# Kernel optimization log

Hardware: AMD Instinct MI355X
Metric: run time of the kernel (lower is better)

Reference implementation:

```python
import jax, jax.numpy as jnp
import numpy as np

# 'tetra_chiral' permutation table from the original module
_TETRA_CHIRAL = np.array([
    [0, 1, 2, 3], [0, 2, 3, 1], [0, 3, 1, 2], [1, 0, 3, 2],
    [1, 2, 0, 3], [1, 3, 2, 0], [2, 0, 1, 3], [2, 1, 3, 0],
    [2, 3, 0, 1], [3, 0, 2, 1], [3, 1, 0, 2], [3, 2, 1, 0]], dtype=np.int32)

N, H = 65536, 256
BN_EPS = 1e-5


def setup_inputs() -> dict:
    key = jax.random.key(0)
    ks = jax.random.split(key, 6)
    x = jax.random.normal(ks[0], (N, 4, H), dtype=jnp.float32)
    # 4 hidden x hidden linears (xavier-ish scale), stacked [4, H, H] (torch weight layout: [out, in])
    Wb = jax.random.normal(ks[1], (4, H, H), dtype=jnp.float32) * (1.0 / np.sqrt(H))
    bb = jnp.zeros((4, H), dtype=jnp.float32)
    W1 = jax.random.normal(ks[2], (H, H), dtype=jnp.float32) * (1.0 / np.sqrt(H))
    b1 = jnp.zeros((H,), dtype=jnp.float32)
    gamma = jnp.ones((H,), dtype=jnp.float32)
    beta = jnp.zeros((H,), dtype=jnp.float32)
    W2 = jax.random.normal(ks[3], (H, H), dtype=jnp.float32) * (1.0 / np.sqrt(H))
    b2 = jnp.zeros((H,), dtype=jnp.float32)
    perms = jnp.asarray(_TETRA_CHIRAL)
    return {"x": x, "Wb": Wb, "bb": bb, "W1": W1, "b1": b1,
            "gamma": gamma, "beta": beta, "W2": W2, "b2": b2, "perms": perms}


def reference(x, Wb, bb, W1, b1, gamma, beta, W2, b2, perms):
    # x: [N, 4, H]; perms: [P, 4] with P=12 (tetra_chiral)
    # For each permutation p: relu(sum_k tanh(Linear_k(x[:, p[k], :]))), accumulated over p.
    acc = jnp.zeros((x.shape[0], perms.shape[0], x.shape[2]), dtype=x.dtype)  # [N, P, H]
    for k in range(4):  # fixed tiny loop over the 4 slot-linears
        xs = x[:, perms[:, k], :]  # gather: [N, P, H]
        acc = acc + jnp.tanh(jnp.einsum('nph,gh->npg', xs, Wb[k]) + bb[k])
    nei = jnp.maximum(acc, 0.0).sum(axis=1)  # relu per perm, sum over perms -> [N, H]
    # mlp_out: Linear -> BatchNorm1d(eval: mean=0, var=1) -> ReLU -> Linear
    z = (nei / 3.0) @ W1.T + b1
    inv = jnp.float32(1.0 / np.sqrt(1.0 + BN_EPS))
    h = jnp.maximum(z * inv * gamma + beta, 0.0)
    return h @ W2.T + b2
```

## Files before the change

### kernel.cpp

```cpp
#include <hip/hip_runtime.h>
#include <cstdint>
#include <cstddef>

typedef __bf16 bf16x8 __attribute__((ext_vector_type(8)));
typedef float  f32x16 __attribute__((ext_vector_type(16)));
typedef float  f32x2  __attribute__((ext_vector_type(2)));

__device__ __forceinline__ unsigned f2bf_u(float f){
  unsigned u = __float_as_uint(f);
  return (u + 0x7FFFu + ((u >> 16) & 1u)) >> 16;
}
__device__ __forceinline__ unsigned short f2bf(float f){ return (unsigned short)f2bf_u(f); }

__device__ __forceinline__ f32x2 tanh2v(f32x2 x){
  f32x2 e2 = x * 2.8853900817779268f;
  f32x2 e  = { __builtin_amdgcn_exp2f(e2.x), __builtin_amdgcn_exp2f(e2.y) };
  f32x2 d  = e + 1.0f;
  f32x2 r  = { __builtin_amdgcn_rcpf(d.x), __builtin_amdgcn_rcpf(d.y) };
  return 1.0f - 2.0f * r;
}

#define MFMA(a,b,c) __builtin_amdgcn_mfma_f32_32x32x16_bf16((a),(b),(c),0,0,0)

__device__ __forceinline__ void ld_lds16(const void* g, void* l){
  __builtin_amdgcn_global_load_lds(
      (const __attribute__((address_space(1))) unsigned int*)g,
      (__attribute__((address_space(3))) unsigned int*)l, 16, 0, 0);
}
__device__ __forceinline__ bf16x8 mk_frag(uint2 lo, uint2 hi){
  return __builtin_bit_cast(bf16x8, make_uint4(lo.x, lo.y, hi.x, hi.y));
}

__global__ void prep_wb(const float* __restrict__ Wb, unsigned short* __restrict__ dst){
  int s  = blockIdx.x*256 + threadIdx.x;
  int r  = s & 31;
  int c  = (s>>5) & 3;
  int tj = (s>>7) & 3;
  int ks = (s>>9) & 3;
  int kq = (s>>11) & 3;
  int gc = (s>>13) & 7;
  const float* src = Wb + ((size_t)tj*256 + gc*32 + r)*256 + kq*64 + ks*16 + c*4;
  float4 f = *reinterpret_cast<const float4*>(src);
  ushort4 o; o.x=f2bf(f.x); o.y=f2bf(f.y); o.z=f2bf(f.z); o.w=f2bf(f.w);
  *reinterpret_cast<ushort4*>(dst + (size_t)s*4) = o;
}

__global__ void prep_w(const float* __restrict__ W1, const float* __restrict__ W2,
                       unsigned short* __restrict__ dst){
  int id = blockIdx.x*256 + threadIdx.x;
  const float* W = (id < 8192) ? W1 : W2;
  int s  = id & 8191;
  int l  = s & 63;
  int ks = (s>>6) & 15;
  int ct = (s>>10) & 7;
  const float* src = W + ((size_t)ct*32 + (l&31))*256 + ks*16 + (l>>5)*8;
  float4 f0 = *reinterpret_cast<const float4*>(src);
  float4 f1 = *reinterpret_cast<const float4*>(src + 4);
  ushort4 a, b;
  a.x=f2bf(f0.x); a.y=f2bf(f0.y); a.z=f2bf(f0.z); a.w=f2bf(f0.w);
  b.x=f2bf(f1.x); b.y=f2bf(f1.y); b.z=f2bf(f1.z); b.w=f2bf(f1.w);
  ushort4* d = reinterpret_cast<ushort4*>(dst + (size_t)id*8);
  d[0] = a; d[1] = b;
}

__launch_bounds__(256, 3)
__global__ void tetra_main(const float* __restrict__ x,
                           const float* __restrict__ bb,
                           const float* __restrict__ b1,
                           const float* __restrict__ gam,
                           const float* __restrict__ bet,
                           const float* __restrict__ b2,
                           const unsigned short* __restrict__ wsWb,
                           const unsigned short* __restrict__ wsW1,
                           const unsigned short* __restrict__ wsW2,
                           float* __restrict__ out)
{
  __shared__ __align__(16) uint2 sbuf[2][2048];
  __shared__ __align__(16) uint2 snei[2112];

  constexpr int PT[12][4] = {{0,1,2,3},{0,2,3,1},{0,3,1,2},{1,0,3,2},{1,2,0,3},{1,3,2,0},
                             {2,0,1,3},{2,1,3,0},{2,3,0,1},{3,0,2,1},{3,1,0,2},{3,2,1,0}};

  const int tid  = threadIdx.x;
  const int w    = tid >> 6;
  const int lane = tid & 63;
  const int l31  = lane & 31;
  const int q    = lane >> 5;

  uint4 fragA[16];
  {
    const float* arow = x + ((size_t)blockIdx.x*128 + (size_t)(w*32 + l31))*256 + q*8;
#pragma unroll
    for (int s = 0; s < 16; ++s){
      float4 f0 = *reinterpret_cast<const float4*>(arow + s*16);
      float4 f1 = *reinterpret_cast<const float4*>(arow + s*16 + 4);
      fragA[s] = make_uint4(f2bf_u(f0.x) | (f2bf_u(f0.y)<<16),
                            f2bf_u(f0.z) | (f2bf_u(f0.w)<<16),
                            f2bf_u(f1.x) | (f2bf_u(f1.y)<<16),
                            f2bf_u(f1.z) | (f2bf_u(f1.w)<<16));
    }
  }

  float bcur[4], bnext[4];
#pragma unroll
  for (int k = 0; k < 4; ++k) bcur[k] = bb[k*256 + l31];

  auto stage = [&](int t){
    const char* g = (const char*)wsWb + (size_t)t*16384 + w*4096 + lane*16;
    char* lb = (char*)(&sbuf[t&1][0]) + w*4096;
#pragma unroll
    for (int i = 0; i < 4; ++i)
      ld_lds16(g + i*1024, lb + i*1024);
  };

  stage(0);

  unsigned short* sn = (unsigned short*)snei;
  int t = 0;
  for (int gc = 0; gc < 8; ++gc){
    f32x16 acc[4];
#pragma unroll
    for (int k = 0; k < 4; ++k){
      float bv = bcur[k];
#pragma unroll
      for (int r = 0; r < 16; ++r) acc[k][r] = bv;
    }

#pragma unroll
    for (int kq = 0; kq < 4; ++kq, ++t){
      __syncthreads();
      if (t < 31) stage(t+1);
      const uint2* B = sbuf[t&1];
      const int boff = q*64 + l31;
#pragma unroll
      for (int ks = 0; ks < 4; ++ks){
        bf16x8 av = __builtin_bit_cast(bf16x8, fragA[kq*4 + ks]);
#pragma unroll
        for (int tj = 0; tj < 4; ++tj){
          int idx = (ks*16 + tj*4)*32 + boff;
          uint2 lo = B[idx], hi = B[idx + 32];
          acc[tj] = MFMA(av, mk_frag(lo, hi), acc[tj]);
        }
      }
    }

#pragma unroll
    for (int k = 0; k < 4; ++k) bnext[k] = bb[k*256 + ((gc+1)&7)*32 + l31];

    const int col   = gc*32 + l31;
    const int sbase = (col>>2)*132 + (col&3);
#pragma unroll
    for (int npair = 0; npair < 2; ++npair){
      const int nb0 = 2*npair, nb1 = nb0 + 1;
      f32x2 th[4][4];
#pragma unroll
      for (int k = 0; k < 4; ++k)
#pragma unroll
        for (int t2 = 0; t2 < 4; ++t2){
          f32x2 a = { acc[k][nb0*4 + t2], acc[k][nb1*4 + t2] };
          th[k][t2] = tanh2v(a);
        }
      float s0 = 0.0f, s1 = 0.0f;
#pragma unroll
      for (int p = 0; p < 12; ++p){
        f32x2 v = (th[0][PT[p][0]] + th[1][PT[p][1]])
                + (th[2][PT[p][2]] + th[3][PT[p][3]]);
        s0 += fmaxf(v.x, 0.0f);
        s1 += fmaxf(v.y, 0.0f);
      }
      sn[sbase + (w*8 + 2*nb0 + q)*4] = f2bf(s0 * (1.0f/3.0f));
      sn[sbase + (w*8 + 2*nb1 + q)*4] = f2bf(s1 * (1.0f/3.0f));
    }

#pragma unroll
    for (int k = 0; k < 4; ++k) bcur[k] = bnext[k];
  }

  float b1v0 = b1[(w*2+0)*32 + l31];
  float b1v1 = b1[(w*2+1)*32 + l31];
  __syncthreads();

  const int ct0 = w*2, ct1 = w*2 + 1;
  f32x16 a2[2];
#pragma unroll
  for (int r = 0; r < 16; ++r){ a2[0][r] = b1v0; a2[1][r] = b1v1; }
  {
    const uint4* W1f = (const uint4*)wsW1;
    uint4 bp[8][2];
#pragma unroll
    for (int i = 0; i < 8; ++i){
      bp[i][0] = W1f[(ct0*16 + i)*64 + lane];
      bp[i][1] = W1f[(ct1*16 + i)*64 + lane];
    }
#pragma unroll
    for (int ks = 0; ks < 16; ++ks){
      int ai = (ks*4 + q*2)*33 + l31;
      uint2 lo = snei[ai], hi = snei[ai + 33];
      bf16x8 av = mk_frag(lo, hi);
      uint4 c0 = bp[ks&7][0], c1 = bp[ks&7][1];
      if (ks < 8){
        bp[ks][0] = W1f[(ct0*16 + ks + 8)*64 + lane];
        bp[ks][1] = W1f[(ct1*16 + ks + 8)*64 + lane];
      }
      a2[0] = MFMA(av, __builtin_bit_cast(bf16x8, c0), a2[0]);
      a2[1] = MFMA(av, __builtin_bit_cast(bf16x8, c1), a2[1]);
    }
  }
  float gvv[2], btv[2], b2v[2];
#pragma unroll
  for (int tj = 0; tj < 2; ++tj){
    int colx = (w*2 + tj)*32 + l31;
    gvv[tj] = gam[colx]; btv[tj] = bet[colx]; b2v[tj] = b2[colx];
  }
  __syncthreads();
  {
    const float inv = 0.9999950000374998f;
#pragma unroll
    for (int tj = 0; tj < 2; ++tj){
      int colx = (w*2 + tj)*32 + l31;
      float gs  = gvv[tj]*inv;
      float btc = btv[tj];
      int cb = (colx>>2)*132 + (colx&3);
#pragma unroll
      for (int r = 0; r < 16; ++r){
        int row = (r&3) + 8*(r>>2) + 4*q;
        sn[cb + row*4] = f2bf(fmaxf(a2[tj][r]*gs + btc, 0.0f));
      }
    }
  }
  __syncthreads();

  f32x16 a3[2];
#pragma unroll
  for (int r = 0; r < 16; ++r){ a3[0][r] = b2v[0]; a3[1][r] = b2v[1]; }
  {
    const uint4* W2f = (const uint4*)wsW2;
    uint4 bp[8][2];
#pragma unroll
    for (int i = 0; i < 8; ++i){
      bp[i][0] = W2f[(ct0*16 + i)*64 + lane];
      bp[i][1] = W2f[(ct1*16 + i)*64 + lane];
    }
#pragma unroll
    for (int ks = 0; ks < 16; ++ks){
      int ai = (ks*4 + q*2)*33 + l31;
      uint2 lo = snei[ai], hi = snei[ai + 33];
      bf16x8 av = mk_frag(lo, hi);
      uint4 c0 = bp[ks&7][0], c1 = bp[ks&7][1];
      if (ks < 8){
        bp[ks][0] = W2f[(ct0*16 + ks + 8)*64 + lane];
        bp[ks][1] = W2f[(ct1*16 + ks + 8)*64 + lane];
      }
      a3[0] = MFMA(av, __builtin_bit_cast(bf16x8, c0), a3[0]);
      a3[1] = MFMA(av, __builtin_bit_cast(bf16x8, c1), a3[1]);
    }
  }
#pragma unroll
  for (int tj = 0; tj < 2; ++tj){
    int colx = (w*2 + tj)*32 + l31;
#pragma unroll
    for (int r = 0; r < 16; ++r){
      int row = (r&3) + 8*(r>>2) + 4*q;
      out[((size_t)blockIdx.x*32 + row)*256 + colx] = a3[tj][r];
    }
  }
}

extern "C" void kernel_launch(void* const* d_in, const int* in_sizes, int n_in,
                              void* d_out, int out_size, void* d_ws, size_t ws_size,
                              hipStream_t stream)
{
  (void)n_in; (void)out_size; (void)ws_size;
  const float* x   = (const float*)d_in[0];
  const float* Wb  = (const float*)d_in[1];
  const float* bb  = (const float*)d_in[2];
  const float* W1  = (const float*)d_in[3];
  const float* b1  = (const float*)d_in[4];
  const float* gam = (const float*)d_in[5];
  const float* bet = (const float*)d_in[6];
  const float* W2  = (const float*)d_in[7];
  const float* b2  = (const float*)d_in[8];
  float* out = (float*)d_out;

  unsigned short* wsWb = (unsigned short*)d_ws;
  unsigned short* wsW1 = wsWb + 262144;
  unsigned short* wsW2 = wsW1 + 65536;

  prep_wb<<<dim3(256), dim3(256), 0, stream>>>(Wb, wsWb);
  prep_w <<<dim3(64),  dim3(256), 0, stream>>>(W1, W2, wsW1);

  const int N = in_sizes[0] / (4*256);
  tetra_main<<<dim3(N/32), dim3(256), 0, stream>>>(x, bb, b1, gam, bet, b2,
                                                   wsWb, wsW1, wsW2, out);
}
```

Baseline: 560.8 us.

## Double block to 512 threads, share staged Wb tiles, swizzle LDS layout

Each block now uses 8 waves and covers 64 tetra items instead of 32. Every Wb tile staged into LDS is therefore reused by twice as many waves, and each wave issues half as many global-to-LDS loads. The Wb prep layout is reordered so each lane's B fragment is a single 16-byte LDS read. The nei/hidden buffer uses an XOR-swizzled layout, and the MLP stage gives each wave one output column tile over two row tiles. The risks are higher register pressure from the 512-thread launch bound and a larger LDS footprint per block.

```diff
diff --git a/kernel.cpp b/kernel.cpp
--- a/kernel.cpp
+++ b/kernel.cpp
@@ -31,15 +31,18 @@
   return __builtin_bit_cast(bf16x8, make_uint4(lo.x, lo.y, hi.x, hi.y));
 }
 
+__device__ __forceinline__ int sslot(int cq, int row){ return cq*64 + (row ^ (cq & 15)); }
+
 __global__ void prep_wb(const float* __restrict__ Wb, unsigned short* __restrict__ dst){
   int s  = blockIdx.x*256 + threadIdx.x;
-  int r  = s & 31;
-  int c  = (s>>5) & 3;
+  int cp = s & 1;
+  int l  = (s>>1) & 63;
   int tj = (s>>7) & 3;
   int ks = (s>>9) & 3;
   int kq = (s>>11) & 3;
   int gc = (s>>13) & 7;
-  const float* src = Wb + ((size_t)tj*256 + gc*32 + r)*256 + kq*64 + ks*16 + c*4;
+  const float* src = Wb + ((size_t)tj*256 + gc*32 + (l&31))*256
+                        + kq*64 + ks*16 + (l>>5)*8 + cp*4;
   float4 f = *reinterpret_cast<const float4*>(src);
   ushort4 o; o.x=f2bf(f.x); o.y=f2bf(f.y); o.z=f2bf(f.z); o.w=f2bf(f.w);
   *reinterpret_cast<ushort4*>(dst + (size_t)s*4) = o;
@@ -63,7 +66,7 @@
   d[0] = a; d[1] = b;
 }
 
-__launch_bounds__(256, 3)
+__launch_bounds__(512, 4)
 __global__ void tetra_main(const float* __restrict__ x,
                            const float* __restrict__ bb,
                            const float* __restrict__ b1,
@@ -76,7 +79,7 @@
                            float* __restrict__ out)
 {
   __shared__ __align__(16) uint2 sbuf[2][2048];
-  __shared__ __align__(16) uint2 snei[2112];
+  __shared__ __align__(16) uint2 snei[4096];
 
   constexpr int PT[12][4] = {{0,1,2,3},{0,2,3,1},{0,3,1,2},{1,0,3,2},{1,2,0,3},{1,3,2,0},
                              {2,0,1,3},{2,1,3,0},{2,3,0,1},{3,0,2,1},{3,1,0,2},{3,2,1,0}};
@@ -89,7 +92,7 @@
 
   uint4 fragA[16];
   {
-    const float* arow = x + ((size_t)blockIdx.x*128 + (size_t)(w*32 + l31))*256 + q*8;
+    const float* arow = x + ((size_t)blockIdx.x*256 + (size_t)(w*32 + l31))*256 + q*8;
 #pragma unroll
     for (int s = 0; s < 16; ++s){
       float4 f0 = *reinterpret_cast<const float4*>(arow + s*16);
@@ -106,10 +109,10 @@
   for (int k = 0; k < 4; ++k) bcur[k] = bb[k*256 + l31];
 
   auto stage = [&](int t){
-    const char* g = (const char*)wsWb + (size_t)t*16384 + w*4096 + lane*16;
-    char* lb = (char*)(&sbuf[t&1][0]) + w*4096;
-#pragma unroll
-    for (int i = 0; i < 4; ++i)
+    const char* g = (const char*)wsWb + (size_t)t*16384 + w*2048 + lane*16;
+    char* lb = (char*)(&sbuf[t&1][0]) + w*2048;
+#pragma unroll
+    for (int i = 0; i < 2; ++i)
       ld_lds16(g + i*1024, lb + i*1024);
   };
 
@@ -130,16 +133,14 @@
     for (int kq = 0; kq < 4; ++kq, ++t){
       __syncthreads();
       if (t < 31) stage(t+1);
-      const uint2* B = sbuf[t&1];
-      const int boff = q*64 + l31;
+      const uint4* B4 = (const uint4*)sbuf[t&1];
 #pragma unroll
       for (int ks = 0; ks < 4; ++ks){
         bf16x8 av = __builtin_bit_cast(bf16x8, fragA[kq*4 + ks]);
 #pragma unroll
         for (int tj = 0; tj < 4; ++tj){
-          int idx = (ks*16 + tj*4)*32 + boff;
-          uint2 lo = B[idx], hi = B[idx + 32];
-          acc[tj] = MFMA(av, mk_frag(lo, hi), acc[tj]);
+          uint4 f = B4[(ks*4 + tj)*64 + lane];
+          acc[tj] = MFMA(av, __builtin_bit_cast(bf16x8, f), acc[tj]);
         }
       }
     }
@@ -147,8 +148,8 @@
 #pragma unroll
     for (int k = 0; k < 4; ++k) bnext[k] = bb[k*256 + ((gc+1)&7)*32 + l31];
 
-    const int col   = gc*32 + l31;
-    const int sbase = (col>>2)*132 + (col&3);
+    const int cq = gc*8 + (l31>>2);
+    const int cl = l31 & 3;
 #pragma unroll
     for (int npair = 0; npair < 2; ++npair){
       const int nb0 = 2*npair, nb1 = nb0 + 1;
@@ -168,102 +169,84 @@
         s0 += fmaxf(v.x, 0.0f);
         s1 += fmaxf(v.y, 0.0f);
       }
-      sn[sbase + (w*8 + 2*nb0 + q)*4] = f2bf(s0 * (1.0f/3.0f));
-      sn[sbase + (w*8 + 2*nb1 + q)*4] = f2bf(s1 * (1.0f/3.0f));
+      sn[sslot(cq, w*8 + 2*nb0 + q)*4 + cl] = f2bf(s0 * (1.0f/3.0f));
+      sn[sslot(cq, w*8 + 2*nb1 + q)*4 + cl] = f2bf(s1 * (1.0f/3.0f));
     }
 
 #pragma unroll
     for (int k = 0; k < 4; ++k) bcur[k] = bnext[k];
   }
 
-  float b1v0 = b1[(w*2+0)*32 + l31];
-  float b1v1 = b1[(w*2+1)*32 + l31];
+  float b1v = b1[w*32 + l31];
   __syncthreads();
 
-  const int ct0 = w*2, ct1 = w*2 + 1;
   f32x16 a2[2];
 #pragma unroll
-  for (int r = 0; r < 16; ++r){ a2[0][r] = b1v0; a2[1][r] = b1v1; }
+  for (int r = 0; r < 16; ++r){ a2[0][r] = b1v; a2[1][r] = b1v; }
   {
     const uint4* W1f = (const uint4*)wsW1;
-    uint4 bp[8][2];
-#pragma unroll
-    for (int i = 0; i < 8; ++i){
-      bp[i][0] = W1f[(ct0*16 + i)*64 + lane];
-      bp[i][1] = W1f[(ct1*16 + i)*64 + lane];
-    }
+    uint4 bp[8];
+#pragma unroll
+    for (int i = 0; i < 8; ++i) bp[i] = W1f[(w*16 + i)*64 + lane];
 #pragma unroll
     for (int ks = 0; ks < 16; ++ks){
-      int ai = (ks*4 + q*2)*33 + l31;
-      uint2 lo = snei[ai], hi = snei[ai + 33];
-      bf16x8 av = mk_frag(lo, hi);
-      uint4 c0 = bp[ks&7][0], c1 = bp[ks&7][1];
-      if (ks < 8){
-        bp[ks][0] = W1f[(ct0*16 + ks + 8)*64 + lane];
-        bp[ks][1] = W1f[(ct1*16 + ks + 8)*64 + lane];
-      }
-      a2[0] = MFMA(av, __builtin_bit_cast(bf16x8, c0), a2[0]);
-      a2[1] = MFMA(av, __builtin_bit_cast(bf16x8, c1), a2[1]);
-    }
-  }
-  float gvv[2], btv[2], b2v[2];
-#pragma unroll
-  for (int tj = 0; tj < 2; ++tj){
-    int colx = (w*2 + tj)*32 + l31;
-    gvv[tj] = gam[colx]; btv[tj] = bet[colx]; b2v[tj] = b2[colx];
-  }
+      uint4 bv = bp[ks&7];
+      if (ks < 8) bp[ks] = W1f[(w*16 + ks + 8)*64 + lane];
+#pragma unroll
+      for (int nr = 0; nr < 2; ++nr){
+        uint2 lo = snei[sslot(ks*4 + q*2,     nr*32 + l31)];
+        uint2 hi = snei[sslot(ks*4 + q*2 + 1, nr*32 + l31)];
+        a2[nr] = MFMA(mk_frag(lo, hi), __builtin_bit_cast(bf16x8, bv), a2[nr]);
+      }
+    }
+  }
+  float gv  = gam[w*32 + l31];
+  float btv = bet[w*32 + l31];
+  float b2v = b2[w*32 + l31];
   __syncthreads();
   {
     const float inv = 0.9999950000374998f;
-#pragma unroll
-    for (int tj = 0; tj < 2; ++tj){
-      int colx = (w*2 + tj)*32 + l31;
-      float gs  = gvv[tj]*inv;
-      float btc = btv[tj];
-      int cb = (colx>>2)*132 + (colx&3);
+    const float gs  = gv * inv;
+    const int   cq  = w*8 + (l31>>2);
+    const int   cl  = l31 & 3;
+#pragma unroll
+    for (int nr = 0; nr < 2; ++nr)
 #pragma unroll
       for (int r = 0; r < 16; ++r){
-        int row = (r&3) + 8*(r>>2) + 4*q;
-        sn[cb + row*4] = f2bf(fmaxf(a2[tj][r]*gs + btc, 0.0f));
-      }
-    }
+        int row = nr*32 + (r&3) + 8*(r>>2) + 4*q;
+        sn[sslot(cq, row)*4 + cl] = f2bf(fmaxf(a2[nr][r]*gs + btv, 0.0f));
+      }
   }
   __syncthreads();
 
   f32x16 a3[2];
 #pragma unroll
-  for (int r = 0; r < 16; ++r){ a3[0][r] = b2v[0]; a3[1][r] = b2v[1]; }
+  for (int r = 0; r < 16; ++r){ a3[0][r] = b2v; a3[1][r] = b2v; }
   {
     const uint4* W2f = (const uint4*)wsW2;
-    uint4 bp[8][2];
-#pragma unroll
-    for (int i = 0; i < 8; ++i){
-      bp[i][0] = W2f[(ct0*16 + i)*64 + lane];
-      bp[i][1] = W2f[(ct1*16 + i)*64 + lane];
-    }
+    uint4 bp[8];
+#pragma unroll
+    for (int i = 0; i < 8; ++i) bp[i] = W2f[(w*16 + i)*64 + lane];
 #pragma unroll
     for (int ks = 0; ks < 16; ++ks){
-      int ai = (ks*4 + q*2)*33 + l31;
-      uint2 lo = snei[ai], hi = snei[ai + 33];
-      bf16x8 av = mk_frag(lo, hi);
-      uint4 c0 = bp[ks&7][0], c1 = bp[ks&7][1];
-      if (ks < 8){
-        bp[ks][0] = W2f[(ct0*16 + ks + 8)*64 + lane];
-        bp[ks][1] = W2f[(ct1*16 + ks + 8)*64 + lane];
-      }
-      a3[0] = MFMA(av, __builtin_bit_cast(bf16x8, c0), a3[0]);
-      a3[1] = MFMA(av, __builtin_bit_cast(bf16x8, c1), a3[1]);
-    }
-  }
-#pragma unroll
-  for (int tj = 0; tj < 2; ++tj){
-    int colx = (w*2 + tj)*32 + l31;
+      uint4 bv = bp[ks&7];
+      if (ks < 8) bp[ks] = W2f[(w*16 + ks + 8)*64 + lane];
+#pragma unroll
+      for (int nr = 0; nr < 2; ++nr){
+        uint2 lo = snei[sslot(ks*4 + q*2,     nr*32 + l31)];
+        uint2 hi = snei[sslot(ks*4 + q*2 + 1, nr*32 + l31)];
+        a3[nr] = MFMA(mk_frag(lo, hi), __builtin_bit_cast(bf16x8, bv), a3[nr]);
+      }
+    }
+  }
+  const int colx = w*32 + l31;
+#pragma unroll
+  for (int nr = 0; nr < 2; ++nr)
 #pragma unroll
     for (int r = 0; r < 16; ++r){
-      int row = (r&3) + 8*(r>>2) + 4*q;
-      out[((size_t)blockIdx.x*32 + row)*256 + colx] = a3[tj][r];
-    }
-  }
+      int row = nr*32 + (r&3) + 8*(r>>2) + 4*q;
+      out[((size_t)blockIdx.x*64 + row)*256 + colx] = a3[nr][r];
+    }
 }
 
 extern "C" void kernel_launch(void* const* d_in, const int* in_sizes, int n_in,
@@ -290,6 +273,6 @@
   prep_w <<<dim3(64),  dim3(256), 0, stream>>>(W1, W2, wsW1);
 
   const int N = in_sizes[0] / (4*256);
-  tetra_main<<<dim3(N/32), dim3(256), 0, stream>>>(x, bb, b1, gam, bet, b2,
+  tetra_main<<<dim3(N/64), dim3(512), 0, stream>>>(x, bb, b1, gam, bet, b2,
                                                    wsWb, wsW1, wsW2, out);
 }
```

Result: slower. 622.2 us (+11.0%).

## Stream Wb fragments directly from global into registers instead of LDS staging

Applied to the files above, without the earlier changes.

Drops the double-buffered LDS staging of the branch weights, along with the per-step block barriers it needed. Each wave now loads its MFMA B fragments straight from global memory (likely L2-resident) into a two-deep register prefetch window. The Wb prep layout is reordered so each lane's 16-byte load matches its MFMA fragment. Occupancy is lowered from 3 to 2 blocks per SU to make room for the extra registers, which trades latency hiding for fewer LDS reads and no synchronization, and every wave now loads the full weights itself.

```diff
diff --git a/kernel.cpp b/kernel.cpp
--- a/kernel.cpp
+++ b/kernel.cpp
@@ -22,24 +22,21 @@
 
 #define MFMA(a,b,c) __builtin_amdgcn_mfma_f32_32x32x16_bf16((a),(b),(c),0,0,0)
 
-__device__ __forceinline__ void ld_lds16(const void* g, void* l){
-  __builtin_amdgcn_global_load_lds(
-      (const __attribute__((address_space(1))) unsigned int*)g,
-      (__attribute__((address_space(3))) unsigned int*)l, 16, 0, 0);
-}
 __device__ __forceinline__ bf16x8 mk_frag(uint2 lo, uint2 hi){
   return __builtin_bit_cast(bf16x8, make_uint4(lo.x, lo.y, hi.x, hi.y));
 }
+__device__ __forceinline__ bf16x8 bc8(uint4 v){ return __builtin_bit_cast(bf16x8, v); }
 
 __global__ void prep_wb(const float* __restrict__ Wb, unsigned short* __restrict__ dst){
   int s  = blockIdx.x*256 + threadIdx.x;
-  int r  = s & 31;
-  int c  = (s>>5) & 3;
+  int cp = s & 1;
+  int l  = (s>>1) & 63;
   int tj = (s>>7) & 3;
   int ks = (s>>9) & 3;
   int kq = (s>>11) & 3;
   int gc = (s>>13) & 7;
-  const float* src = Wb + ((size_t)tj*256 + gc*32 + r)*256 + kq*64 + ks*16 + c*4;
+  const float* src = Wb + ((size_t)tj*256 + gc*32 + (l&31))*256
+                        + kq*64 + ks*16 + (l>>5)*8 + cp*4;
   float4 f = *reinterpret_cast<const float4*>(src);
   ushort4 o; o.x=f2bf(f.x); o.y=f2bf(f.y); o.z=f2bf(f.z); o.w=f2bf(f.w);
   *reinterpret_cast<ushort4*>(dst + (size_t)s*4) = o;
@@ -63,7 +60,7 @@
   d[0] = a; d[1] = b;
 }
 
-__launch_bounds__(256, 3)
+__launch_bounds__(256, 2)
 __global__ void tetra_main(const float* __restrict__ x,
                            const float* __restrict__ bb,
                            const float* __restrict__ b1,
@@ -75,7 +72,6 @@
                            const unsigned short* __restrict__ wsW2,
                            float* __restrict__ out)
 {
-  __shared__ __align__(16) uint2 sbuf[2][2048];
   __shared__ __align__(16) uint2 snei[2112];
 
   constexpr int PT[12][4] = {{0,1,2,3},{0,2,3,1},{0,3,1,2},{1,0,3,2},{1,2,0,3},{1,3,2,0},
@@ -105,18 +101,14 @@
 #pragma unroll
   for (int k = 0; k < 4; ++k) bcur[k] = bb[k*256 + l31];
 
-  auto stage = [&](int t){
-    const char* g = (const char*)wsWb + (size_t)t*16384 + w*4096 + lane*16;
-    char* lb = (char*)(&sbuf[t&1][0]) + w*4096;
-#pragma unroll
-    for (int i = 0; i < 4; ++i)
-      ld_lds16(g + i*1024, lb + i*1024);
-  };
-
-  stage(0);
+  const uint4* Wf = (const uint4*)wsWb;
+  uint4 win[2][4];
+#pragma unroll
+  for (int tj = 0; tj < 4; ++tj) win[0][tj] = Wf[(0*4 + tj)*64 + lane];
+#pragma unroll
+  for (int tj = 0; tj < 4; ++tj) win[1][tj] = Wf[(1*4 + tj)*64 + lane];
 
   unsigned short* sn = (unsigned short*)snei;
-  int t = 0;
   for (int gc = 0; gc < 8; ++gc){
     f32x16 acc[4];
 #pragma unroll
@@ -126,21 +118,26 @@
       for (int r = 0; r < 16; ++r) acc[k][r] = bv;
     }
 
-#pragma unroll
-    for (int kq = 0; kq < 4; ++kq, ++t){
-      __syncthreads();
-      if (t < 31) stage(t+1);
-      const uint2* B = sbuf[t&1];
-      const int boff = q*64 + l31;
+    const int gbase = gc*16;
+#pragma unroll
+    for (int kq = 0; kq < 4; ++kq){
 #pragma unroll
       for (int ks = 0; ks < 4; ++ks){
-        bf16x8 av = __builtin_bit_cast(bf16x8, fragA[kq*4 + ks]);
-#pragma unroll
-        for (int tj = 0; tj < 4; ++tj){
-          int idx = (ks*16 + tj*4)*32 + boff;
-          uint2 lo = B[idx], hi = B[idx + 32];
-          acc[tj] = MFMA(av, mk_frag(lo, hi), acc[tj]);
+        constexpr int JJ = 0;
+        (void)JJ;
+        const int j = kq*4 + ks;
+        bf16x8 av = bc8(fragA[j]);
+        uint4 c0 = win[j&1][0], c1 = win[j&1][1], c2 = win[j&1][2], c3 = win[j&1][3];
+        if (j < 14 || gc < 7){
+          const int gp = gbase + j + 2;
+#pragma unroll
+          for (int tj = 0; tj < 4; ++tj)
+            win[j&1][tj] = Wf[(gp*4 + tj)*64 + lane];
         }
+        acc[0] = MFMA(av, bc8(c0), acc[0]);
+        acc[1] = MFMA(av, bc8(c1), acc[1]);
+        acc[2] = MFMA(av, bc8(c2), acc[2]);
+        acc[3] = MFMA(av, bc8(c3), acc[3]);
       }
     }
 
@@ -202,8 +199,8 @@
         bp[ks][0] = W1f[(ct0*16 + ks + 8)*64 + lane];
         bp[ks][1] = W1f[(ct1*16 + ks + 8)*64 + lane];
       }
-      a2[0] = MFMA(av, __builtin_bit_cast(bf16x8, c0), a2[0]);
-      a2[1] = MFMA(av, __builtin_bit_cast(bf16x8, c1), a2[1]);
+      a2[0] = MFMA(av, bc8(c0), a2[0]);
+      a2[1] = MFMA(av, bc8(c1), a2[1]);
     }
   }
   float gvv[2], btv[2], b2v[2];
@@ -251,8 +248,8 @@
         bp[ks][0] = W2f[(ct0*16 + ks + 8)*64 + lane];
         bp[ks][1] = W2f[(ct1*16 + ks + 8)*64 + lane];
       }
-      a3[0] = MFMA(av, __builtin_bit_cast(bf16x8, c0), a3[0]);
-      a3[1] = MFMA(av, __builtin_bit_cast(bf16x8, c1), a3[1]);
+      a3[0] = MFMA(av, bc8(c0), a3[0]);
+      a3[1] = MFMA(av, bc8(c1), a3[1]);
     }
   }
 #pragma unroll
```

Result: slower. 655.2 us (+16.8%).
